# Performance work log

Hardware: AMD Instinct MI355X
Metric: run time of the kernel (lower is better)

Reference implementation:

```python
import jax, jax.numpy as jnp
import numpy as np

WS = 8
NH = 6

def setup_inputs() -> dict:
    key = jax.random.key(0)
    ks = jax.random.split(key, 6)
    B, H, W, C = 4, 256, 256, 192
    return {
        "x": jax.random.normal(ks[0], (B, H * W, C), dtype=jnp.float32),
        "qkv_w": jax.random.normal(ks[1], (3 * C, C), dtype=jnp.float32) * 0.02,
        "qkv_b": jax.random.normal(ks[2], (3 * C,), dtype=jnp.float32) * 0.02,
        "proj_w": jax.random.normal(ks[3], (C, C), dtype=jnp.float32) * 0.02,
        "proj_b": jax.random.normal(ks[4], (C,), dtype=jnp.float32) * 0.02,
        "bias": jax.random.normal(ks[5], (NH, WS * WS, WS * WS), dtype=jnp.float32) * 0.02,
        "H": H,
        "W": W,
    }

def reference(x, qkv_w, qkv_b, proj_w, proj_b, bias, H, W):
    B, L, C = x.shape
    ws, nh = WS, NH
    hd = C // nh
    scale = hd ** -0.5
    H_pad = (H + ws - 1) // ws * ws
    W_pad = (W + ws - 1) // ws * ws
    pad_b, pad_r = H_pad - H, W_pad - W
    xv = x.reshape(B, H, W, C)
    if pad_b > 0 or pad_r > 0:
        xv = jnp.pad(xv, ((0, 0), (0, pad_b), (0, pad_r), (0, 0)))
    nHw, nWw = H_pad // ws, W_pad // ws
    # window partition: [B*nH*nW, ws*ws, C]
    xw = xv.reshape(B, nHw, ws, nWw, ws, C).transpose(0, 1, 3, 2, 4, 5)
    xw = xw.reshape(B * nHw * nWw, ws * ws, C)
    qkv = xw @ qkv_w.T + qkv_b  # [Bw, ws*ws, 3C]
    qkv = qkv.reshape(-1, ws * ws, 3, nh, hd).transpose(2, 0, 3, 1, 4)
    q, k, v = qkv[0], qkv[1], qkv[2]  # each [Bw, nh, ws*ws, hd]
    attn = jnp.einsum('bhqd,bhkd->bhqk', q * scale, k) + bias
    attn = jax.nn.softmax(attn, axis=-1)
    out = jnp.einsum('bhqk,bhkd->bhqd', attn, v)
    out = out.transpose(0, 2, 1, 3).reshape(-1, ws * ws, C)
    out = out @ proj_w.T + proj_b
    # window reverse: [B, H_pad, W_pad, C]
    out = out.reshape(B, nHw, nWw, ws, ws, C).transpose(0, 1, 3, 2, 4, 5)
    out = out.reshape(B, H_pad, W_pad, C)
    if pad_b > 0 or pad_r > 0:
        out = out[:, :H, :W, :]
    return out.reshape(B, H * W, C)
```

## Files before the change

kernel.cpp:

```cpp
#include <hip/hip_runtime.h>

typedef short bf16x8 __attribute__((ext_vector_type(8)));
typedef float f32x4 __attribute__((ext_vector_type(4)));

#define QKV_FRAG_SH 110592
#define PROJ_FRAG_SH 36864
#define BIAS2_OFF_B 294912
#define SCALE 0.17677669529663689f
#define LOG2E 1.44269504088896341f
#define QSCALE (SCALE * LOG2E)
#define SMEM_BYTES 161792

__device__ __forceinline__ short f2bf(float f) {
  unsigned x = __float_as_uint(f);
  x = (x + 0x7FFFu + ((x >> 16) & 1u)) >> 16;
  return (short)x;
}

__global__ void cvt_w(const float* __restrict__ qkv_w,
                      const float* __restrict__ proj_w,
                      const float* __restrict__ bias,
                      short* __restrict__ wfrag,
                      float* __restrict__ bias2) {
  int idx = blockIdx.x * 256 + threadIdx.x;
  if (idx < QKV_FRAG_SH) {
    int j = idx & 7, lane = (idx >> 3) & 63, t = idx >> 9;
    int nt = t / 6, ks = t - nt * 6;
    int n0 = nt * 16 + (lane & 15);
    float v = qkv_w[n0 * 192 + ks * 32 + (lane >> 4) * 8 + j];
    if (n0 < 192) v *= QSCALE;
    wfrag[idx] = f2bf(v);
  } else if (idx < QKV_FRAG_SH + PROJ_FRAG_SH) {
    int i2 = idx - QKV_FRAG_SH;
    int j = i2 & 7, lane = (i2 >> 3) & 63, t = i2 >> 9;
    int nt = t / 6, ks = t - nt * 6;
    wfrag[idx] = f2bf(proj_w[(nt * 16 + (lane & 15)) * 192 + ks * 32 + (lane >> 4) * 8 + j]);
  } else {
    int i3 = idx - (QKV_FRAG_SH + PROJ_FRAG_SH);
    bias2[i3] = bias[i3] * LOG2E;
  }
}

__global__ __launch_bounds__(768, 3) void swin_fused(
    const float* __restrict__ x,
    const float* __restrict__ qkv_b,
    const float* __restrict__ proj_b,
    const short* __restrict__ wfrag,
    const float* __restrict__ bias2,
    float* __restrict__ out) {
  extern __shared__ short smem[];
  short* buf = smem;
  short* q_l = smem + 25600;
  short* k_l = smem + 39424;
  short* v_l = smem + 53248;
  short* p_s = smem + 67072;

  const short* wq = wfrag;
  const short* wp = wfrag + QKV_FRAG_SH;

  const int tid = threadIdx.x;
  const int w = tid >> 6, lane = tid & 63, quad = lane >> 4, lm = lane & 15;
  const int m = w & 3, g = w >> 2;

  int goff[4], loff[4];
  #pragma unroll
  for (int i = 0; i < 4; ++i) {
    int idx4 = tid + i * 768;
    int chunk = idx4 / 384;
    int off = idx4 - chunk * 384;
    goff[i] = chunk * 49152 + off * 4;
    loff[i] = (chunk * 8 + off / 48) * 200 + (off % 48) * 4;
  }

  size_t base;
  {
    int wid = blockIdx.x;
    int b = wid >> 10, rem = wid & 1023, wh = rem >> 5, ww = rem & 31;
    base = ((size_t)b * 65536 + (size_t)(wh * 8) * 256 + (size_t)(ww * 8)) * 192;
    const float* xp = x + base;
    #pragma unroll
    for (int i = 0; i < 4; ++i) {
      float4 f = *(const float4*)(xp + goff[i]);
      short4 s = { f2bf(f.x), f2bf(f.y), f2bf(f.z), f2bf(f.w) };
      *(short4*)&buf[loff[i]] = s;
    }
  }
  __syncthreads();

  float4 pf[4];
  size_t nbase = 0;
  #pragma unroll 1
  for (int it = 0; it < 16; ++it) {
    const int cur = (it & 1) * 12800;
    const int nxt = 12800 - cur;

    if (it < 15) {
      int wid = (it + 1) * 256 + blockIdx.x;
      int b = wid >> 10, rem = wid & 1023, wh = rem >> 5, ww = rem & 31;
      nbase = ((size_t)b * 65536 + (size_t)(wh * 8) * 256 + (size_t)(ww * 8)) * 192;
      const float* xp = x + nbase;
      #pragma unroll
      for (int i = 0; i < 4; ++i) pf[i] = *(const float4*)(xp + goff[i]);
    }

    {
      bf16x8 af[6];
      #pragma unroll
      for (int ks = 0; ks < 6; ++ks)
        af[ks] = *(const bf16x8*)&buf[cur + (m * 16 + lm) * 200 + ks * 32 + quad * 8];
      const int nt0 = g * 12;
      for (int ntl = 0; ntl < 12; ++ntl) {
        int nt = nt0 + ntl;
        f32x4 acc = {0.f, 0.f, 0.f, 0.f};
        #pragma unroll
        for (int ks = 0; ks < 6; ++ks) {
          bf16x8 bw = *(const bf16x8*)&wq[((nt * 6 + ks) * 64 + lane) * 8];
          acc = __builtin_amdgcn_mfma_f32_16x16x32_bf16(af[ks], bw, acc, 0, 0, 0);
        }
        float bn = qkv_b[nt * 16 + lm];
        if (nt < 12) {
          bn *= QSCALE;
          int h = nt >> 1, dh = nt & 1;
          int rb = h * 64 + m * 16 + quad * 4;
          #pragma unroll
          for (int r = 0; r < 4; ++r)
            q_l[(rb + r) * 36 + dh * 16 + lm] = f2bf(acc[r] + bn);
        } else if (nt < 24) {
          int h = (nt - 12) >> 1, dh = nt & 1;
          int rb = h * 64 + m * 16 + quad * 4;
          #pragma unroll
          for (int r = 0; r < 4; ++r)
            k_l[(rb + r) * 36 + dh * 16 + lm] = f2bf(acc[r] + bn);
        } else {
          int h = (nt - 24) >> 1, dh = nt & 1;
          short4 s4 = { f2bf(acc[0] + bn), f2bf(acc[1] + bn),
                        f2bf(acc[2] + bn), f2bf(acc[3] + bn) };
          *(short4*)&v_l[(h * 32 + dh * 16 + lm) * 72 + m * 16 + quad * 4] = s4;
        }
      }
    }
    __syncthreads();

    if (it < 15) {
      #pragma unroll
      for (int i = 0; i < 4; ++i) {
        short4 s = { f2bf(pf[i].x), f2bf(pf[i].y), f2bf(pf[i].z), f2bf(pf[i].w) };
        *(short4*)&buf[nxt + loff[i]] = s;
      }
    }

    {
      const int pb = w * 1152;
      #pragma unroll 1
      for (int i = 0; i < 2; ++i) {
        int tk = w + i * 12;
        int h = tk >> 2, mt = tk & 3;
        const float* bp = bias2 + h * 4096 + (mt * 16 + quad * 4) * 64 + lm;
        f32x4 lg[4];
        #pragma unroll
        for (int nt = 0; nt < 4; ++nt) {
          lg[nt][0] = bp[nt * 16];
          lg[nt][1] = bp[nt * 16 + 64];
          lg[nt][2] = bp[nt * 16 + 128];
          lg[nt][3] = bp[nt * 16 + 192];
        }
        bf16x8 aq = *(const bf16x8*)&q_l[(h * 64 + mt * 16 + lm) * 36 + quad * 8];
        #pragma unroll
        for (int nt = 0; nt < 4; ++nt) {
          bf16x8 bk = *(const bf16x8*)&k_l[(h * 64 + nt * 16 + lm) * 36 + quad * 8];
          lg[nt] = __builtin_amdgcn_mfma_f32_16x16x32_bf16(aq, bk, lg[nt], 0, 0, 0);
        }
        float s[4] = {0.f, 0.f, 0.f, 0.f};
        #pragma unroll
        for (int r = 0; r < 4; ++r) {
          #pragma unroll
          for (int nt = 0; nt < 4; ++nt) {
            float e = exp2f(lg[nt][r]);
            s[r] += e;
            p_s[pb + (quad * 4 + r) * 72 + nt * 16 + lm] = f2bf(e);
          }
        }
        #pragma unroll
        for (int r = 0; r < 4; ++r) {
          s[r] += __shfl_xor(s[r], 1);
          s[r] += __shfl_xor(s[r], 2);
          s[r] += __shfl_xor(s[r], 4);
          s[r] += __shfl_xor(s[r], 8);
        }
        asm volatile("s_waitcnt lgkmcnt(0)" ::: "memory");
        f32x4 o0 = {0.f,0.f,0.f,0.f}, o1 = {0.f,0.f,0.f,0.f};
        #pragma unroll
        for (int ks = 0; ks < 2; ++ks) {
          bf16x8 ap  = *(const bf16x8*)&p_s[pb + lm * 72 + ks * 32 + quad * 8];
          bf16x8 bv0 = *(const bf16x8*)&v_l[(h * 32 + lm) * 72 + ks * 32 + quad * 8];
          bf16x8 bv1 = *(const bf16x8*)&v_l[(h * 32 + 16 + lm) * 72 + ks * 32 + quad * 8];
          o0 = __builtin_amdgcn_mfma_f32_16x16x32_bf16(ap, bv0, o0, 0, 0, 0);
          o1 = __builtin_amdgcn_mfma_f32_16x16x32_bf16(ap, bv1, o1, 0, 0, 0);
        }
        #pragma unroll
        for (int r = 0; r < 4; ++r) {
          float ir = 1.0f / s[r];
          int rowo = cur + (mt * 16 + quad * 4 + r) * 200 + h * 32;
          buf[rowo + lm]      = f2bf(o0[r] * ir);
          buf[rowo + 16 + lm] = f2bf(o1[r] * ir);
        }
      }
    }
    __syncthreads();

    {
      bf16x8 af2[6];
      #pragma unroll
      for (int ks = 0; ks < 6; ++ks)
        af2[ks] = *(const bf16x8*)&buf[cur + (m * 16 + lm) * 200 + ks * 32 + quad * 8];
      const int nt0 = g * 4;
      #pragma unroll 1
      for (int ntl = 0; ntl < 4; ++ntl) {
        int nt = nt0 + ntl;
        f32x4 acc = {0.f, 0.f, 0.f, 0.f};
        #pragma unroll
        for (int ks = 0; ks < 6; ++ks) {
          bf16x8 bw = *(const bf16x8*)&wp[((nt * 6 + ks) * 64 + lane) * 8];
          acc = __builtin_amdgcn_mfma_f32_16x16x32_bf16(af2[ks], bw, acc, 0, 0, 0);
        }
        float pbv = proj_b[nt * 16 + lm];
        #pragma unroll
        for (int r = 0; r < 4; ++r) {
          int t = m * 16 + quad * 4 + r;
          out[base + (size_t)((t >> 3) * 256 + (t & 7)) * 192 + nt * 16 + lm] = acc[r] + pbv;
        }
      }
    }
    base = nbase;
  }
}

extern "C" void kernel_launch(void* const* d_in, const int* in_sizes, int n_in,
                              void* d_out, int out_size, void* d_ws, size_t ws_size,
                              hipStream_t stream) {
  const float* x      = (const float*)d_in[0];
  const float* qkv_w  = (const float*)d_in[1];
  const float* qkv_b  = (const float*)d_in[2];
  const float* proj_w = (const float*)d_in[3];
  const float* proj_b = (const float*)d_in[4];
  const float* bias   = (const float*)d_in[5];
  short* wfrag = (short*)d_ws;
  float* bias2 = (float*)((char*)d_ws + BIAS2_OFF_B);

  hipFuncSetAttribute((const void*)swin_fused,
                      hipFuncAttributeMaxDynamicSharedMemorySize, SMEM_BYTES);

  hipLaunchKernelGGL(cvt_w, dim3(672), dim3(256), 0, stream,
                     qkv_w, proj_w, bias, wfrag, bias2);
  hipLaunchKernelGGL(swin_fused, dim3(256), dim3(768), SMEM_BYTES, stream,
                     x, qkv_b, proj_b, wfrag, bias2, (float*)d_out);
}
```

Measured before the change: 573.1 us.

## Retile QKV and proj GEMMs so each weight fragment feeds all four row tiles

Each wave in the QKV GEMM now computes 3 column tiles across all 4 row tiles, and in the projection it computes 1 column tile across all 4 row tiles. Each global weight fragment load is therefore reused by four MFMAs instead of one. Biases are folded into the accumulator initialisation, and the qkv bias is prescaled in the conversion kernel. The attention bias is pre-permuted into MFMA fragment order so it can be read with vectorised f32x4 loads. The trade-off is a larger accumulator set (48 floats), which raises register pressure under the 768-thread launch bound.

```diff
diff --git a/kernel.cpp b/kernel.cpp
--- a/kernel.cpp
+++ b/kernel.cpp
@@ -6,6 +6,7 @@
 #define QKV_FRAG_SH 110592
 #define PROJ_FRAG_SH 36864
 #define BIAS2_OFF_B 294912
+#define QKVB2_OFF_B 393216
 #define SCALE 0.17677669529663689f
 #define LOG2E 1.44269504088896341f
 #define QSCALE (SCALE * LOG2E)
@@ -20,8 +21,10 @@
 __global__ void cvt_w(const float* __restrict__ qkv_w,
                       const float* __restrict__ proj_w,
                       const float* __restrict__ bias,
+                      const float* __restrict__ qkv_b,
                       short* __restrict__ wfrag,
-                      float* __restrict__ bias2) {
+                      float* __restrict__ bias2,
+                      float* __restrict__ qkvb2) {
   int idx = blockIdx.x * 256 + threadIdx.x;
   if (idx < QKV_FRAG_SH) {
     int j = idx & 7, lane = (idx >> 3) & 63, t = idx >> 9;
@@ -35,18 +38,24 @@
     int j = i2 & 7, lane = (i2 >> 3) & 63, t = i2 >> 9;
     int nt = t / 6, ks = t - nt * 6;
     wfrag[idx] = f2bf(proj_w[(nt * 16 + (lane & 15)) * 192 + ks * 32 + (lane >> 4) * 8 + j]);
-  } else {
+  } else if (idx < QKV_FRAG_SH + PROJ_FRAG_SH + 24576) {
     int i3 = idx - (QKV_FRAG_SH + PROJ_FRAG_SH);
-    bias2[i3] = bias[i3] * LOG2E;
+    int r = i3 & 3, nt = (i3 >> 2) & 3, lane = (i3 >> 4) & 63, mt = (i3 >> 10) & 3, h = i3 >> 12;
+    int row = mt * 16 + (lane >> 4) * 4 + r;
+    int col = nt * 16 + (lane & 15);
+    bias2[i3] = bias[h * 4096 + row * 64 + col] * LOG2E;
+  } else if (idx < QKV_FRAG_SH + PROJ_FRAG_SH + 24576 + 576) {
+    int i4 = idx - (QKV_FRAG_SH + PROJ_FRAG_SH + 24576);
+    qkvb2[i4] = qkv_b[i4] * (i4 < 192 ? QSCALE : 1.0f);
   }
 }
 
 __global__ __launch_bounds__(768, 3) void swin_fused(
     const float* __restrict__ x,
-    const float* __restrict__ qkv_b,
     const float* __restrict__ proj_b,
     const short* __restrict__ wfrag,
     const float* __restrict__ bias2,
+    const float* __restrict__ qkvb2,
     float* __restrict__ out) {
   extern __shared__ short smem[];
   short* buf = smem;
@@ -60,7 +69,6 @@
 
   const int tid = threadIdx.x;
   const int w = tid >> 6, lane = tid & 63, quad = lane >> 4, lm = lane & 15;
-  const int m = w & 3, g = w >> 2;
 
   int goff[4], loff[4];
   #pragma unroll
@@ -104,38 +112,62 @@
     }
 
     {
-      bf16x8 af[6];
-      #pragma unroll
-      for (int ks = 0; ks < 6; ++ks)
-        af[ks] = *(const bf16x8*)&buf[cur + (m * 16 + lm) * 200 + ks * 32 + quad * 8];
-      const int nt0 = g * 12;
-      for (int ntl = 0; ntl < 12; ++ntl) {
-        int nt = nt0 + ntl;
-        f32x4 acc = {0.f, 0.f, 0.f, 0.f};
-        #pragma unroll
-        for (int ks = 0; ks < 6; ++ks) {
-          bf16x8 bw = *(const bf16x8*)&wq[((nt * 6 + ks) * 64 + lane) * 8];
-          acc = __builtin_amdgcn_mfma_f32_16x16x32_bf16(af[ks], bw, acc, 0, 0, 0);
-        }
-        float bn = qkv_b[nt * 16 + lm];
-        if (nt < 12) {
-          bn *= QSCALE;
-          int h = nt >> 1, dh = nt & 1;
-          int rb = h * 64 + m * 16 + quad * 4;
-          #pragma unroll
-          for (int r = 0; r < 4; ++r)
-            q_l[(rb + r) * 36 + dh * 16 + lm] = f2bf(acc[r] + bn);
-        } else if (nt < 24) {
-          int h = (nt - 12) >> 1, dh = nt & 1;
-          int rb = h * 64 + m * 16 + quad * 4;
-          #pragma unroll
-          for (int r = 0; r < 4; ++r)
-            k_l[(rb + r) * 36 + dh * 16 + lm] = f2bf(acc[r] + bn);
-        } else {
-          int h = (nt - 24) >> 1, dh = nt & 1;
-          short4 s4 = { f2bf(acc[0] + bn), f2bf(acc[1] + bn),
-                        f2bf(acc[2] + bn), f2bf(acc[3] + bn) };
-          *(short4*)&v_l[(h * 32 + dh * 16 + lm) * 72 + m * 16 + quad * 4] = s4;
+      const int nt0 = w * 3;
+      f32x4 acc[3][4];
+      #pragma unroll
+      for (int j = 0; j < 3; ++j) {
+        float bn = qkvb2[(nt0 + j) * 16 + lm];
+        #pragma unroll
+        for (int mm = 0; mm < 4; ++mm) acc[j][mm] = (f32x4){bn, bn, bn, bn};
+      }
+      #pragma unroll 2
+      for (int ks = 0; ks < 6; ++ks) {
+        bf16x8 a[4];
+        #pragma unroll
+        for (int mm = 0; mm < 4; ++mm)
+          a[mm] = *(const bf16x8*)&buf[cur + (mm * 16 + lm) * 200 + ks * 32 + quad * 8];
+        #pragma unroll
+        for (int j = 0; j < 3; ++j) {
+          bf16x8 bwf = *(const bf16x8*)&wq[((nt0 + j) * 6 + ks) * 512 + lane * 8];
+          #pragma unroll
+          for (int mm = 0; mm < 4; ++mm)
+            acc[j][mm] = __builtin_amdgcn_mfma_f32_16x16x32_bf16(a[mm], bwf, acc[j][mm], 0, 0, 0);
+        }
+      }
+      if (w < 4) {
+        #pragma unroll
+        for (int j = 0; j < 3; ++j) {
+          int nt = nt0 + j, h = nt >> 1, dh = nt & 1;
+          #pragma unroll
+          for (int mm = 0; mm < 4; ++mm) {
+            int rb = h * 64 + mm * 16 + quad * 4;
+            #pragma unroll
+            for (int r = 0; r < 4; ++r)
+              q_l[(rb + r) * 36 + dh * 16 + lm] = f2bf(acc[j][mm][r]);
+          }
+        }
+      } else if (w < 8) {
+        #pragma unroll
+        for (int j = 0; j < 3; ++j) {
+          int nt = nt0 + j, h = (nt - 12) >> 1, dh = nt & 1;
+          #pragma unroll
+          for (int mm = 0; mm < 4; ++mm) {
+            int rb = h * 64 + mm * 16 + quad * 4;
+            #pragma unroll
+            for (int r = 0; r < 4; ++r)
+              k_l[(rb + r) * 36 + dh * 16 + lm] = f2bf(acc[j][mm][r]);
+          }
+        }
+      } else {
+        #pragma unroll
+        for (int j = 0; j < 3; ++j) {
+          int nt = nt0 + j, h = (nt - 24) >> 1, dh = nt & 1;
+          #pragma unroll
+          for (int mm = 0; mm < 4; ++mm) {
+            short4 s4 = { f2bf(acc[j][mm][0]), f2bf(acc[j][mm][1]),
+                          f2bf(acc[j][mm][2]), f2bf(acc[j][mm][3]) };
+            *(short4*)&v_l[(h * 32 + dh * 16 + lm) * 72 + mm * 16 + quad * 4] = s4;
+          }
         }
       }
     }
@@ -155,15 +187,11 @@
       for (int i = 0; i < 2; ++i) {
         int tk = w + i * 12;
         int h = tk >> 2, mt = tk & 3;
-        const float* bp = bias2 + h * 4096 + (mt * 16 + quad * 4) * 64 + lm;
+        const float* bp = bias2 + ((h * 4 + mt) * 64 + lane) * 16;
         f32x4 lg[4];
         #pragma unroll
-        for (int nt = 0; nt < 4; ++nt) {
-          lg[nt][0] = bp[nt * 16];
-          lg[nt][1] = bp[nt * 16 + 64];
-          lg[nt][2] = bp[nt * 16 + 128];
-          lg[nt][3] = bp[nt * 16 + 192];
-        }
+        for (int nt = 0; nt < 4; ++nt)
+          lg[nt] = *(const f32x4*)(bp + nt * 4);
         bf16x8 aq = *(const bf16x8*)&q_l[(h * 64 + mt * 16 + lm) * 36 + quad * 8];
         #pragma unroll
         for (int nt = 0; nt < 4; ++nt) {
@@ -209,25 +237,26 @@
     __syncthreads();
 
     {
-      bf16x8 af2[6];
-      #pragma unroll
-      for (int ks = 0; ks < 6; ++ks)
-        af2[ks] = *(const bf16x8*)&buf[cur + (m * 16 + lm) * 200 + ks * 32 + quad * 8];
-      const int nt0 = g * 4;
-      #pragma unroll 1
-      for (int ntl = 0; ntl < 4; ++ntl) {
-        int nt = nt0 + ntl;
-        f32x4 acc = {0.f, 0.f, 0.f, 0.f};
-        #pragma unroll
-        for (int ks = 0; ks < 6; ++ks) {
-          bf16x8 bw = *(const bf16x8*)&wp[((nt * 6 + ks) * 64 + lane) * 8];
-          acc = __builtin_amdgcn_mfma_f32_16x16x32_bf16(af2[ks], bw, acc, 0, 0, 0);
-        }
-        float pbv = proj_b[nt * 16 + lm];
-        #pragma unroll
-        for (int r = 0; r < 4; ++r) {
-          int t = m * 16 + quad * 4 + r;
-          out[base + (size_t)((t >> 3) * 256 + (t & 7)) * 192 + nt * 16 + lm] = acc[r] + pbv;
+      const int nt = w;
+      float pbv = proj_b[nt * 16 + lm];
+      f32x4 acc[4];
+      #pragma unroll
+      for (int mm = 0; mm < 4; ++mm) acc[mm] = (f32x4){pbv, pbv, pbv, pbv};
+      #pragma unroll 2
+      for (int ks = 0; ks < 6; ++ks) {
+        bf16x8 bwf = *(const bf16x8*)&wp[(nt * 6 + ks) * 512 + lane * 8];
+        #pragma unroll
+        for (int mm = 0; mm < 4; ++mm) {
+          bf16x8 am = *(const bf16x8*)&buf[cur + (mm * 16 + lm) * 200 + ks * 32 + quad * 8];
+          acc[mm] = __builtin_amdgcn_mfma_f32_16x16x32_bf16(am, bwf, acc[mm], 0, 0, 0);
+        }
+      }
+      #pragma unroll
+      for (int mm = 0; mm < 4; ++mm) {
+        #pragma unroll
+        for (int r = 0; r < 4; ++r) {
+          int t = mm * 16 + quad * 4 + r;
+          out[base + (size_t)((t >> 3) * 256 + (t & 7)) * 192 + nt * 16 + lm] = acc[mm][r];
         }
       }
     }
@@ -246,12 +275,13 @@
   const float* bias   = (const float*)d_in[5];
   short* wfrag = (short*)d_ws;
   float* bias2 = (float*)((char*)d_ws + BIAS2_OFF_B);
+  float* qkvb2 = (float*)((char*)d_ws + QKVB2_OFF_B);
 
   hipFuncSetAttribute((const void*)swin_fused,
                       hipFuncAttributeMaxDynamicSharedMemorySize, SMEM_BYTES);
 
-  hipLaunchKernelGGL(cvt_w, dim3(672), dim3(256), 0, stream,
-                     qkv_w, proj_w, bias, wfrag, bias2);
+  hipLaunchKernelGGL(cvt_w, dim3(675), dim3(256), 0, stream,
+                     qkv_w, proj_w, bias, qkv_b, wfrag, bias2, qkvb2);
   hipLaunchKernelGGL(swin_fused, dim3(256), dim3(768), SMEM_BYTES, stream,
-                     x, qkv_b, proj_b, wfrag, bias2, (float*)d_out);
-}
+                     x, proj_b, wfrag, bias2, qkvb2, (float*)d_out);
+}
```

Measured after the change: 543.2 us. 1.05x faster.
